# Kernel optimization log

Hardware: AMD Instinct MI355X
Metric: run time of the kernel (lower is better)

## Reference

```python
import jax, jax.numpy as jnp
import numpy as np
import math

B, S, H, NH = 2, 2048, 1024, 16
DK = H // NH


def setup_inputs() -> dict:
    key = jax.random.key(0)
    k1, k2, k3 = jax.random.split(key, 3)
    scale = 1.0 / math.sqrt(H)
    return {
        "x": jax.random.normal(k1, (B, S, H), dtype=jnp.float32),
        "w_attn": jax.random.normal(k2, (H, 3 * H), dtype=jnp.float32) * scale,
        "b_attn": jnp.zeros((3 * H,), dtype=jnp.float32),
        "w_proj": jax.random.normal(k3, (H, H), dtype=jnp.float32) * scale,
        "b_proj": jnp.zeros((H,), dtype=jnp.float32),
    }


def reference(x, w_attn, b_attn, w_proj, b_proj):
    bs, seq_len, hidden = x.shape
    qkv = x @ w_attn + b_attn                       # [B,S,3H]
    q, k, v = jnp.split(qkv, 3, axis=-1)
    # [B,S,H] -> [B,NH,S,DK]
    def heads(t):
        return t.reshape(bs, seq_len, NH, DK).transpose(0, 2, 1, 3)
    q, k, v = heads(q), heads(k), heads(v)
    scores = jnp.einsum('bhqd,bhkd->bhqk', q, k) / math.sqrt(DK)  # [B,NH,S,S]
    causal = jnp.tril(jnp.ones((seq_len, seq_len), dtype=bool))
    scores = jnp.where(causal[None, None], scores, -jnp.inf)
    attn = jax.nn.softmax(scores, axis=-1)
    out = jnp.einsum('bhqk,bhkd->bhqd', attn, v)    # [B,NH,S,DK]
    out = out.transpose(0, 2, 1, 3).reshape(bs, seq_len, hidden)
    return out @ w_proj + b_proj
```

## Files before the change

kernel.cpp:

```cpp
#include <hip/hip_runtime.h>

#define BATCH 2
#define S_LEN 2048
#define NHEADS 16
#define DKV 64
#define HID 1024

typedef __attribute__((ext_vector_type(8))) short s16x8;
typedef __attribute__((ext_vector_type(4))) short s16x4;
typedef __attribute__((ext_vector_type(4))) float f32x4;

__device__ inline unsigned short f2bf(float f) {
    union { float f; unsigned int u; } v; v.f = f;
    unsigned int r = v.u + 0x7fffu + ((v.u >> 16) & 1u);
    return (unsigned short)(r >> 16);
}

__device__ inline s16x8 pack8(float4 a, float4 b) {
    s16x8 r;
    r[0] = (short)f2bf(a.x); r[1] = (short)f2bf(a.y);
    r[2] = (short)f2bf(a.z); r[3] = (short)f2bf(a.w);
    r[4] = (short)f2bf(b.x); r[5] = (short)f2bf(b.y);
    r[6] = (short)f2bf(b.z); r[7] = (short)f2bf(b.w);
    return r;
}

__device__ inline void gload_lds16(const void* g, void* l) {
    __builtin_amdgcn_global_load_lds(
        (const __attribute__((address_space(1))) void*)g,
        (__attribute__((address_space(3))) void*)l, 16, 0, 0);
}

__global__ __launch_bounds__(256)
void f32_to_bf16_kernel(const float* __restrict__ in, unsigned short* __restrict__ out, int n8) {
    int i = blockIdx.x * 256 + threadIdx.x;
    if (i < n8) {
        const float4* p = (const float4*)(in + (size_t)i * 8);
        float4 a = p[0], b = p[1];
        *(s16x8*)(out + (size_t)i * 8) = pack8(a, b);
    }
}

__global__ __launch_bounds__(256)
void transpose_bf16_kernel(const float* __restrict__ in, unsigned short* __restrict__ out,
                           int K, int N) {
    __shared__ float tile[32][33];
    int n0 = blockIdx.x * 32;
    int k0 = blockIdx.y * 32;
    int tx = threadIdx.x, ty = threadIdx.y;
    for (int i = ty; i < 32; i += 8)
        tile[i][tx] = in[(size_t)(k0 + i) * N + n0 + tx];
    __syncthreads();
    for (int i = ty; i < 32; i += 8)
        out[(size_t)(n0 + i) * K + k0 + tx] = f2bf(tile[tx][i]);
}

__global__ __launch_bounds__(256)
void gemm_qkv_kernel(const unsigned short* __restrict__ A, const unsigned short* __restrict__ Bt,
                     const float* __restrict__ bias, unsigned short* __restrict__ qkv,
                     unsigned short* __restrict__ vT, int M, int N, int K) {
    __shared__ __align__(16) unsigned short As[128 * 64];
    __shared__ __align__(16) unsigned short Bs[128 * 64];

    const int tid  = threadIdx.x;
    const int lane = tid & 63;
    const int wv   = tid >> 6;
    const int wr   = wv >> 1, wc = wv & 1;
    const int m0   = blockIdx.y * 128, n0 = blockIdx.x * 128;

    const int lr = lane & 15;
    const int lg = lane >> 4;

    const int srow = lane >> 3;
    const int scol = ((lane & 7) ^ srow) * 8;

    f32x4 acc[4][4] = {};

    for (int k0 = 0; k0 < K; k0 += 64) {
        __syncthreads();
        #pragma unroll
        for (int l = 0; l < 4; l++) {
            const int r0 = wv * 32 + l * 8;
            gload_lds16(A  + (size_t)(m0 + r0 + srow) * K + k0 + scol, &As[r0 * 64]);
            gload_lds16(Bt + (size_t)(n0 + r0 + srow) * K + k0 + scol, &Bs[r0 * 64]);
        }
        __syncthreads();

        #pragma unroll
        for (int kk = 0; kk < 2; kk++) {
            s16x8 af[4], bfr[4];
            #pragma unroll
            for (int mi = 0; mi < 4; mi++)
                af[mi] = *(const s16x8*)&As[(wr * 64 + mi * 16 + lr) * 64 + (((kk * 4 + lg) ^ (lr & 7)) * 8)];
            #pragma unroll
            for (int ni = 0; ni < 4; ni++)
                bfr[ni] = *(const s16x8*)&Bs[(wc * 64 + ni * 16 + lr) * 64 + (((kk * 4 + lg) ^ (lr & 7)) * 8)];
            #pragma unroll
            for (int mi = 0; mi < 4; mi++)
                #pragma unroll
                for (int ni = 0; ni < 4; ni++)
                    acc[mi][ni] = __builtin_amdgcn_mfma_f32_16x16x32_bf16(af[mi], bfr[ni], acc[mi][ni], 0, 0, 0);
        }
    }

    const bool isV = (n0 >= 2 * HID);
    #pragma unroll
    for (int mi = 0; mi < 4; mi++) {
        #pragma unroll
        for (int ni = 0; ni < 4; ni++) {
            int col = n0 + wc * 64 + ni * 16 + lr;
            float bv = bias[col];
            int row0 = m0 + wr * 64 + mi * 16 + lg * 4;
            if (isV) {
                int d = col - 2 * HID;
                int bb = row0 >> 11;
                int s = row0 & (S_LEN - 1);
                s16x4 pk;
                #pragma unroll
                for (int r = 0; r < 4; r++)
                    pk[r] = (short)f2bf(acc[mi][ni][r] + bv);
                *(s16x4*)&vT[((size_t)bb * HID + d) * S_LEN + s] = pk;
            } else {
                #pragma unroll
                for (int r = 0; r < 4; r++)
                    qkv[(size_t)(row0 + r) * N + col] = f2bf(acc[mi][ni][r] + bv);
            }
        }
    }
}

__global__ __launch_bounds__(256)
void gemm64_kernel(const unsigned short* __restrict__ A, const unsigned short* __restrict__ Bt,
                   const float* __restrict__ bias, float* __restrict__ Cout,
                   int M, int N, int K) {
    __shared__ __align__(16) unsigned short As[64 * 32];
    __shared__ __align__(16) unsigned short Bs[128 * 32];

    const int tid  = threadIdx.x;
    const int lane = tid & 63;
    const int wv   = tid >> 6;
    const int wr   = wv >> 1, wc = wv & 1;
    const int m0   = blockIdx.y * 64, n0 = blockIdx.x * 128;

    const int lr = lane & 15;
    const int lg = lane >> 4;
    const int lk = lg * 8;

    const int srow = lane >> 2;
    const int scol = (lane & 3) * 8;

    const int arow = tid >> 2;
    const int acol = (tid & 3) * 8;

    f32x4 acc[2][4] = {};

    for (int k0 = 0; k0 < K; k0 += 32) {
        __syncthreads();
        gload_lds16(A + (size_t)(m0 + arow) * K + k0 + acol, &As[(arow & ~3) * 32]);
        #pragma unroll
        for (int l = 0; l < 2; l++) {
            const int r0 = wv * 32 + l * 16;
            gload_lds16(Bt + (size_t)(n0 + r0 + srow) * K + k0 + scol, &Bs[r0 * 32]);
        }
        __syncthreads();

        s16x8 af[2], bfr[4];
        #pragma unroll
        for (int mi = 0; mi < 2; mi++)
            af[mi] = *(const s16x8*)&As[(wr * 32 + mi * 16 + lr) * 32 + lk];
        #pragma unroll
        for (int ni = 0; ni < 4; ni++)
            bfr[ni] = *(const s16x8*)&Bs[(wc * 64 + ni * 16 + lr) * 32 + lk];
        #pragma unroll
        for (int mi = 0; mi < 2; mi++)
            #pragma unroll
            for (int ni = 0; ni < 4; ni++)
                acc[mi][ni] = __builtin_amdgcn_mfma_f32_16x16x32_bf16(af[mi], bfr[ni], acc[mi][ni], 0, 0, 0);
    }

    #pragma unroll
    for (int mi = 0; mi < 2; mi++) {
        #pragma unroll
        for (int ni = 0; ni < 4; ni++) {
            int col = n0 + wc * 64 + ni * 16 + lr;
            float bv = bias[col];
            #pragma unroll
            for (int r = 0; r < 4; r++) {
                int row = m0 + wr * 32 + mi * 16 + lg * 4 + r;
                Cout[(size_t)row * N + col] = acc[mi][ni][r] + bv;
            }
        }
    }
}

__global__ __launch_bounds__(256)
void attn_kernel(const unsigned short* __restrict__ qkv, const unsigned short* __restrict__ vT,
                 unsigned short* __restrict__ out) {
    __shared__ __align__(16) unsigned short Ks[2][64 * 64];
    __shared__ __align__(16) unsigned short Vs[2][64 * 64];
    __shared__ __align__(16) unsigned short Ps[4][16][72];

    const int tid  = threadIdx.x;
    const int lane = tid & 63;
    const int w    = tid >> 6;
    const int head = blockIdx.y;
    const int b    = blockIdx.z;

    const size_t rowbase = (size_t)b * S_LEN;
    const int hoff = head * DKV;

    const int lr = lane & 15;
    const int lg = lane >> 4;
    const int lk = lg * 8;

    const int krow   = lane >> 3;
    const int kchunk = ((lane & 7) ^ krow) * 8;

    s16x8 onesA;
    #pragma unroll
    for (int i = 0; i < 8; i++) onesA[i] = (lr == 0) ? (short)0x3F80 : (short)0;

    #pragma unroll
    for (int panel = 0; panel < 2; panel++) {
        const int qb = (panel == 0) ? (int)blockIdx.x : (31 - (int)blockIdx.x);
        const int q0 = qb * 64;
        const int nt = qb + 1;

        s16x8 qf[2];
        {
            const unsigned short* qp = qkv + (rowbase + q0 + w * 16 + lr) * (3 * HID) + hoff;
            qf[0] = *(const s16x8*)(qp + lk);
            qf[1] = *(const s16x8*)(qp + 32 + lk);
        }

        f32x4 o[4] = {};
        f32x4 l4 = {};
        int cur = 0;

        __syncthreads();
        #pragma unroll
        for (int l = 0; l < 2; l++) {
            const int r0 = (w * 2 + l) * 8;
            gload_lds16(qkv + (rowbase + r0 + krow) * (3 * HID) + HID + hoff + kchunk,
                        &Ks[0][r0 * 64]);
            gload_lds16(vT + ((size_t)b * HID + hoff + r0 + krow) * S_LEN + kchunk,
                        &Vs[0][r0 * 64]);
        }

        for (int tt = 0; tt < nt; tt++) {
            __syncthreads();

            if (tt + 1 < nt) {
                const int jn = (tt + 1) * 64;
                #pragma unroll
                for (int l = 0; l < 2; l++) {
                    const int r0 = (w * 2 + l) * 8;
                    gload_lds16(qkv + (rowbase + jn + r0 + krow) * (3 * HID) + HID + hoff + kchunk,
                                &Ks[cur ^ 1][r0 * 64]);
                    gload_lds16(vT + ((size_t)b * HID + hoff + r0 + krow) * S_LEN + jn + kchunk,
                                &Vs[cur ^ 1][r0 * 64]);
                }
            }

            f32x4 sf[4] = {};
            #pragma unroll
            for (int kt = 0; kt < 2; kt++)
                #pragma unroll
                for (int ni = 0; ni < 4; ni++) {
                    s16x8 kb = *(const s16x8*)&Ks[cur][(ni * 16 + lr) * 64 + (((kt * 4 + lg) ^ (lr & 7)) * 8)];
                    sf[ni] = __builtin_amdgcn_mfma_f32_16x16x32_bf16(qf[kt], kb, sf[ni], 0, 0, 0);
                }

            const bool diag = (tt == nt - 1);
            #pragma unroll
            for (int ni = 0; ni < 4; ni++) {
                #pragma unroll
                for (int r = 0; r < 4; r++) {
                    float s = sf[ni][r];
                    if (diag) {
                        int qi = w * 16 + lg * 4 + r;
                        if (ni * 16 + lr > qi) s = -INFINITY;
                    }
                    float pv = exp2f(__fmaf_rn(s, 0.18033688f, -17.3123405f));
                    union { float f; unsigned int u; } cv; cv.f = pv;
                    Ps[w][lg * 4 + r][ni * 16 + lr] = (unsigned short)(cv.u >> 16);
                }
            }

            #pragma unroll
            for (int kt = 0; kt < 2; kt++) {
                s16x8 pa = *(const s16x8*)&Ps[w][lr][kt * 32 + lk];
                #pragma unroll
                for (int dt = 0; dt < 4; dt++) {
                    s16x8 vb = *(const s16x8*)&Vs[cur][(dt * 16 + lr) * 64 + (((kt * 4 + lg) ^ (lr & 7)) * 8)];
                    o[dt] = __builtin_amdgcn_mfma_f32_16x16x32_bf16(vb, pa, o[dt], 0, 0, 0);
                }
                l4 = __builtin_amdgcn_mfma_f32_16x16x32_bf16(onesA, pa, l4, 0, 0, 0);
            }
            cur ^= 1;
        }

        {
            float invl = 1.0f / __shfl(l4[0], lr);
            int qrow = q0 + w * 16 + lr;
            #pragma unroll
            for (int dt = 0; dt < 4; dt++) {
                s16x4 pk;
                #pragma unroll
                for (int r = 0; r < 4; r++) pk[r] = (short)f2bf(o[dt][r] * invl);
                *(s16x4*)&out[(rowbase + qrow) * HID + hoff + dt * 16 + lg * 4] = pk;
            }
        }
    }
}

extern "C" void kernel_launch(void* const* d_in, const int* in_sizes, int n_in,
                              void* d_out, int out_size, void* d_ws, size_t ws_size,
                              hipStream_t stream) {
    const float* x      = (const float*)d_in[0];
    const float* w_attn = (const float*)d_in[1];
    const float* b_attn = (const float*)d_in[2];
    const float* w_proj = (const float*)d_in[3];
    const float* b_proj = (const float*)d_in[4];
    float* out = (float*)d_out;

    char* ws = (char*)d_ws;
    unsigned short* qkv      = (unsigned short*)(ws);
    unsigned short* waT      = (unsigned short*)(ws + 25165824);
    unsigned short* wpT      = (unsigned short*)(ws + 31457280);
    unsigned short* attn_out = (unsigned short*)(ws + 33554432);
    unsigned short* xb       = (unsigned short*)(ws + 41943040);
    unsigned short* vTr      = (unsigned short*)(ws + 50331648);

    const int M = BATCH * S_LEN;

    f32_to_bf16_kernel<<<dim3((M * HID / 8 + 255) / 256), 256, 0, stream>>>(x, xb, M * HID / 8);

    dim3 tb(32, 8);
    transpose_bf16_kernel<<<dim3(3 * HID / 32, HID / 32), tb, 0, stream>>>(w_attn, waT, HID, 3 * HID);
    transpose_bf16_kernel<<<dim3(HID / 32, HID / 32), tb, 0, stream>>>(w_proj, wpT, HID, HID);

    gemm_qkv_kernel<<<dim3(3 * HID / 128, M / 128), 256, 0, stream>>>(
        xb, waT, b_attn, qkv, vTr, M, 3 * HID, HID);

    attn_kernel<<<dim3(16, NHEADS, BATCH), 256, 0, stream>>>(qkv, vTr, attn_out);

    gemm64_kernel<<<dim3(HID / 128, M / 64), 256, 0, stream>>>(
        attn_out, wpT, b_proj, out, M, HID, HID);
}
```

Before: 129.4 us.

## Keep attention probabilities in registers via transposed scores and lane shuffles

The attention kernel now computes transposed score tiles (K as the A operand), so each lane holds probabilities for one query row. These are packed to bf16 with v_cvt_pk_bf16_f32 and redistributed with cross-lane shuffles into the P operand layout. This replaces the shared-memory P staging and the extra ones-vector MFMA used for row sums, which are now a register sum plus xor-shuffle reduction. The V transpose moves out of the QKV GEMM epilogue into a separate transpose kernel, which adds a launch and an extra read/write of V in exchange for simpler, uniform GEMM stores.

```diff
diff --git a/kernel.cpp b/kernel.cpp
--- a/kernel.cpp
+++ b/kernel.cpp
@@ -29,6 +29,12 @@
     __builtin_amdgcn_global_load_lds(
         (const __attribute__((address_space(1))) void*)g,
         (__attribute__((address_space(3))) void*)l, 16, 0, 0);
+}
+
+__device__ inline unsigned int cvtpk_bf16(float lo, float hi) {
+    unsigned int d;
+    asm("v_cvt_pk_bf16_f32 %0, %1, %2" : "=v"(d) : "v"(lo), "v"(hi));
+    return d;
 }
 
 __global__ __launch_bounds__(256)
@@ -56,9 +62,24 @@
 }
 
 __global__ __launch_bounds__(256)
+void vtrans_kernel(const unsigned short* __restrict__ qkv, unsigned short* __restrict__ vT) {
+    __shared__ unsigned short tile[32][33];
+    int c0 = blockIdx.x * 32;
+    int s0 = blockIdx.y * 32;
+    int b  = blockIdx.z;
+    int tx = threadIdx.x, ty = threadIdx.y;
+    const size_t rowbase = (size_t)b * S_LEN;
+    for (int i = ty; i < 32; i += 8)
+        tile[i][tx] = qkv[(rowbase + s0 + i) * (3 * HID) + 2 * HID + c0 + tx];
+    __syncthreads();
+    for (int i = ty; i < 32; i += 8)
+        vT[((size_t)b * HID + c0 + i) * S_LEN + s0 + tx] = tile[tx][i];
+}
+
+__global__ __launch_bounds__(256)
 void gemm_qkv_kernel(const unsigned short* __restrict__ A, const unsigned short* __restrict__ Bt,
                      const float* __restrict__ bias, unsigned short* __restrict__ qkv,
-                     unsigned short* __restrict__ vT, int M, int N, int K) {
+                     int M, int N, int K) {
     __shared__ __align__(16) unsigned short As[128 * 64];
     __shared__ __align__(16) unsigned short Bs[128 * 64];
 
@@ -103,7 +124,6 @@
         }
     }
 
-    const bool isV = (n0 >= 2 * HID);
     #pragma unroll
     for (int mi = 0; mi < 4; mi++) {
         #pragma unroll
@@ -111,20 +131,9 @@
             int col = n0 + wc * 64 + ni * 16 + lr;
             float bv = bias[col];
             int row0 = m0 + wr * 64 + mi * 16 + lg * 4;
-            if (isV) {
-                int d = col - 2 * HID;
-                int bb = row0 >> 11;
-                int s = row0 & (S_LEN - 1);
-                s16x4 pk;
-                #pragma unroll
-                for (int r = 0; r < 4; r++)
-                    pk[r] = (short)f2bf(acc[mi][ni][r] + bv);
-                *(s16x4*)&vT[((size_t)bb * HID + d) * S_LEN + s] = pk;
-            } else {
-                #pragma unroll
-                for (int r = 0; r < 4; r++)
-                    qkv[(size_t)(row0 + r) * N + col] = f2bf(acc[mi][ni][r] + bv);
-            }
+            #pragma unroll
+            for (int r = 0; r < 4; r++)
+                qkv[(size_t)(row0 + r) * N + col] = f2bf(acc[mi][ni][r] + bv);
         }
     }
 }
@@ -198,7 +207,6 @@
                  unsigned short* __restrict__ out) {
     __shared__ __align__(16) unsigned short Ks[2][64 * 64];
     __shared__ __align__(16) unsigned short Vs[2][64 * 64];
-    __shared__ __align__(16) unsigned short Ps[4][16][72];
 
     const int tid  = threadIdx.x;
     const int lane = tid & 63;
@@ -216,10 +224,6 @@
     const int krow   = lane >> 3;
     const int kchunk = ((lane & 7) ^ krow) * 8;
 
-    s16x8 onesA;
-    #pragma unroll
-    for (int i = 0; i < 8; i++) onesA[i] = (lr == 0) ? (short)0x3F80 : (short)0;
-
     #pragma unroll
     for (int panel = 0; panel < 2; panel++) {
         const int qb = (panel == 0) ? (int)blockIdx.x : (31 - (int)blockIdx.x);
@@ -234,7 +238,7 @@
         }
 
         f32x4 o[4] = {};
-        f32x4 l4 = {};
+        float lsum = 0.0f;
         int cur = 0;
 
         __syncthreads();
@@ -262,54 +266,63 @@
                 }
             }
 
-            f32x4 sf[4] = {};
+            f32x4 sfT[4] = {};
             #pragma unroll
             for (int kt = 0; kt < 2; kt++)
                 #pragma unroll
                 for (int ni = 0; ni < 4; ni++) {
                     s16x8 kb = *(const s16x8*)&Ks[cur][(ni * 16 + lr) * 64 + (((kt * 4 + lg) ^ (lr & 7)) * 8)];
-                    sf[ni] = __builtin_amdgcn_mfma_f32_16x16x32_bf16(qf[kt], kb, sf[ni], 0, 0, 0);
+                    sfT[ni] = __builtin_amdgcn_mfma_f32_16x16x32_bf16(kb, qf[kt], sfT[ni], 0, 0, 0);
                 }
 
             const bool diag = (tt == nt - 1);
+            unsigned int own[4][2];
             #pragma unroll
             for (int ni = 0; ni < 4; ni++) {
+                float pv[4];
                 #pragma unroll
                 for (int r = 0; r < 4; r++) {
-                    float s = sf[ni][r];
+                    float s = sfT[ni][r];
                     if (diag) {
-                        int qi = w * 16 + lg * 4 + r;
-                        if (ni * 16 + lr > qi) s = -INFINITY;
+                        int kl = ni * 16 + lg * 4 + r;
+                        if (kl > w * 16 + lr) s = -INFINITY;
                     }
-                    float pv = exp2f(__fmaf_rn(s, 0.18033688f, -17.3123405f));
-                    union { float f; unsigned int u; } cv; cv.f = pv;
-                    Ps[w][lg * 4 + r][ni * 16 + lr] = (unsigned short)(cv.u >> 16);
-                }
+                    pv[r] = exp2f(__fmaf_rn(s, 0.18033688f, -17.3123405f));
+                }
+                lsum += (pv[0] + pv[1]) + (pv[2] + pv[3]);
+                own[ni][0] = cvtpk_bf16(pv[0], pv[1]);
+                own[ni][1] = cvtpk_bf16(pv[2], pv[3]);
             }
 
             #pragma unroll
             for (int kt = 0; kt < 2; kt++) {
-                s16x8 pa = *(const s16x8*)&Ps[w][lr][kt * 32 + lk];
+                union { int u[4]; s16x8 v; } pa;
+                #pragma unroll
+                for (int c = 0; c < 4; c++) {
+                    int srcLane = ((lg & 1) * 2 + (c >> 1)) * 16 + lr;
+                    int r1 = __shfl((int)own[kt * 2 + 0][c & 1], srcLane, 64);
+                    int r2 = __shfl((int)own[kt * 2 + 1][c & 1], srcLane, 64);
+                    pa.u[c] = (lg >= 2) ? r2 : r1;
+                }
                 #pragma unroll
                 for (int dt = 0; dt < 4; dt++) {
                     s16x8 vb = *(const s16x8*)&Vs[cur][(dt * 16 + lr) * 64 + (((kt * 4 + lg) ^ (lr & 7)) * 8)];
-                    o[dt] = __builtin_amdgcn_mfma_f32_16x16x32_bf16(vb, pa, o[dt], 0, 0, 0);
-                }
-                l4 = __builtin_amdgcn_mfma_f32_16x16x32_bf16(onesA, pa, l4, 0, 0, 0);
+                    o[dt] = __builtin_amdgcn_mfma_f32_16x16x32_bf16(vb, pa.v, o[dt], 0, 0, 0);
+                }
             }
             cur ^= 1;
         }
 
-        {
-            float invl = 1.0f / __shfl(l4[0], lr);
-            int qrow = q0 + w * 16 + lr;
-            #pragma unroll
-            for (int dt = 0; dt < 4; dt++) {
-                s16x4 pk;
-                #pragma unroll
-                for (int r = 0; r < 4; r++) pk[r] = (short)f2bf(o[dt][r] * invl);
-                *(s16x4*)&out[(rowbase + qrow) * HID + hoff + dt * 16 + lg * 4] = pk;
-            }
+        lsum += __shfl_xor(lsum, 16, 64);
+        lsum += __shfl_xor(lsum, 32, 64);
+        float invl = 1.0f / lsum;
+        int qrow = q0 + w * 16 + lr;
+        #pragma unroll
+        for (int dt = 0; dt < 4; dt++) {
+            s16x4 pk;
+            #pragma unroll
+            for (int r = 0; r < 4; r++) pk[r] = (short)f2bf(o[dt][r] * invl);
+            *(s16x4*)&out[(rowbase + qrow) * HID + hoff + dt * 16 + lg * 4] = pk;
         }
     }
 }
@@ -341,7 +354,9 @@
     transpose_bf16_kernel<<<dim3(HID / 32, HID / 32), tb, 0, stream>>>(w_proj, wpT, HID, HID);
 
     gemm_qkv_kernel<<<dim3(3 * HID / 128, M / 128), 256, 0, stream>>>(
-        xb, waT, b_attn, qkv, vTr, M, 3 * HID, HID);
+        xb, waT, b_attn, qkv, M, 3 * HID, HID);
+
+    vtrans_kernel<<<dim3(HID / 32, S_LEN / 32, BATCH), tb, 0, stream>>>(qkv, vTr);
 
     attn_kernel<<<dim3(16, NHEADS, BATCH), 256, 0, stream>>>(qkv, vTr, attn_out);
 
```

Result: slower. 143.4 us (+10.9%).
